# Kernel optimization log

Hardware: AMD Instinct MI355X
Metric: run time of the kernel (lower is better)

## Reference

```python
import jax, jax.numpy as jnp
import numpy as np

N = 100000   # nodes
E = 800000   # edges
P = 100000   # pos/neg pairs
H = 4        # heads
IN = 128     # input feature dim
HID = 32     # per-head out dim (H*HID = 128)


def gat_layer(h, src, dst, W, al, ar, b):
    """DGL-style GATConv: gather -> leaky_relu attention -> segment softmax -> scatter."""
    n = h.shape[0]
    nh, nf = al.shape
    feat = (h @ W).reshape(n, nh, nf)                       # [N,H,F]
    el = jnp.einsum('nhf,hf->nh', feat, al)                 # [N,H]
    er = jnp.einsum('nhf,hf->nh', feat, ar)                 # [N,H]
    e = jax.nn.leaky_relu(el[src] + er[dst], negative_slope=0.2)  # [E,H]
    emax = jax.ops.segment_max(e, dst, num_segments=n)      # [N,H]
    emax = jnp.where(jnp.isfinite(emax), emax, 0.0)         # zero-in-degree guard
    w = jnp.exp(e - emax[dst])                              # [E,H]
    denom = jax.ops.segment_sum(w, dst, num_segments=n)     # [N,H]
    alpha = w / jnp.maximum(denom[dst], 1e-9)               # [E,H]
    out = jax.ops.segment_sum(feat[src] * alpha[:, :, None], dst, num_segments=n)  # [N,H,F]
    return out.reshape(n, nh * nf) + b


def setup_inputs() -> dict:
    key = jax.random.key(0)
    ks = jax.random.split(key, 32)
    s = 0.1
    d = {
        'x': jax.random.normal(ks[0], (N, IN), jnp.float32),
        'src': jax.random.randint(ks[1], (E,), 0, N),
        'dst': jax.random.randint(ks[2], (E,), 0, N),
        'pos_src': jax.random.randint(ks[3], (P,), 0, N),
        'pos_dst': jax.random.randint(ks[4], (P,), 0, N),
        'neg_src': jax.random.randint(ks[5], (P,), 0, N),
        'neg_dst': jax.random.randint(ks[6], (P,), 0, N),
    }
    HF = H * HID
    # 3 GATConv layers, all 128 -> 4x32
    for l in range(3):
        ind = IN if l == 0 else HF
        d[f'W{l}'] = s * jax.random.normal(ks[7 + 4 * l], (ind, HF), jnp.float32)
        d[f'al{l}'] = s * jax.random.normal(ks[8 + 4 * l], (H, HID), jnp.float32)
        d[f'ar{l}'] = s * jax.random.normal(ks[9 + 4 * l], (H, HID), jnp.float32)
        d[f'b{l}'] = jnp.zeros((HF,), jnp.float32)
    # projection 128 -> 32
    d['Wp'] = s * jax.random.normal(ks[20], (HF, HID), jnp.float32)
    d['bp'] = jnp.zeros((HID,), jnp.float32)
    # predictor MLP 32 -> 32 -> 32 -> 1
    d['Wq1'] = s * jax.random.normal(ks[21], (HID, HID), jnp.float32)
    d['bq1'] = jnp.zeros((HID,), jnp.float32)
    d['Wq2'] = s * jax.random.normal(ks[22], (HID, HID), jnp.float32)
    d['bq2'] = jnp.zeros((HID,), jnp.float32)
    d['Wq3'] = s * jax.random.normal(ks[23], (HID, 1), jnp.float32)
    d['bq3'] = jnp.zeros((1,), jnp.float32)
    return d


def reference(x, src, dst, pos_src, pos_dst, neg_src, neg_dst,
              W0, al0, ar0, b0, W1, al1, ar1, b1, W2, al2, ar2, b2,
              Wp, bp, Wq1, bq1, Wq2, bq2, Wq3, bq3):
    h = x
    for W, al, ar, b in ((W0, al0, ar0, b0), (W1, al1, ar1, b1), (W2, al2, ar2, b2)):
        h = jax.nn.elu(gat_layer(h, src, dst, W, al, ar, b))
    h = h @ Wp + bp                                          # [N,HID]

    def predictor(z):
        z = jax.nn.relu(z @ Wq1 + bq1)
        z = jax.nn.relu(z @ Wq2 + bq2)
        return z @ Wq3 + bq3

    h_pos = predictor(h[pos_src] * h[pos_dst])               # [P,1]
    h_neg = predictor(h[neg_src] * h[neg_dst])               # [P,1]
    return (h_pos, h_neg)
```

## Files before the change

kernel.cpp:

```cpp
#include <hip/hip_runtime.h>
#include <math.h>

typedef __attribute__((ext_vector_type(8))) short bf16x8;
typedef __attribute__((ext_vector_type(4))) float f32x4;

__device__ __forceinline__ unsigned short f2bf_rtne(float v) {
    unsigned u = __float_as_uint(v);
    u += 0x7FFFu + ((u >> 16) & 1u);
    return (unsigned short)(u >> 16);
}

__global__ __launch_bounds__(256) void hist_k(const int* __restrict__ dst, int* __restrict__ deg, int e) {
    int i4 = (blockIdx.x * 256 + threadIdx.x) * 4;
    if (i4 + 3 < e) {
        int4 d = *(const int4*)(dst + i4);
        atomicAdd(&deg[d.x], 1);
        atomicAdd(&deg[d.y], 1);
        atomicAdd(&deg[d.z], 1);
        atomicAdd(&deg[d.w], 1);
    } else {
        for (int j = i4; j < e; j++) atomicAdd(&deg[dst[j]], 1);
    }
}

__global__ __launch_bounds__(256) void scan1_k(const int* __restrict__ deg, int* __restrict__ rowptr,
                                               int* __restrict__ bsum, int n) {
    __shared__ int sh[256];
    int tid = threadIdx.x;
    int sid = blockIdx.x * 256 + tid;
    int v = (sid < n) ? deg[sid] : 0;
    sh[tid] = v; __syncthreads();
    for (int off = 1; off < 256; off <<= 1) {
        int t = (tid >= off) ? sh[tid - off] : 0;
        __syncthreads();
        sh[tid] += t;
        __syncthreads();
    }
    if (sid < n) rowptr[sid + 1] = sh[tid];
    if (tid == 255) bsum[blockIdx.x] = sh[255];
}

__global__ __launch_bounds__(512) void scan2_k(int* __restrict__ bsum, int nb) {
    __shared__ int sh[512];
    int tid = threadIdx.x;
    sh[tid] = (tid < nb) ? bsum[tid] : 0;
    __syncthreads();
    for (int off = 1; off < 512; off <<= 1) {
        int t = (tid >= off) ? sh[tid - off] : 0;
        __syncthreads();
        sh[tid] += t;
        __syncthreads();
    }
    if (tid < nb) bsum[tid] = sh[tid];
}

__global__ __launch_bounds__(256) void scan3_k(int* __restrict__ rowptr, int* __restrict__ cursor,
                                               const int* __restrict__ bsum, int n) {
    int sid = blockIdx.x * 256 + threadIdx.x;
    if (sid == 0) { rowptr[0] = 0; cursor[0] = 0; }
    if (sid < n) {
        int v = rowptr[sid + 1];
        if (blockIdx.x > 0) v += bsum[blockIdx.x - 1];
        rowptr[sid + 1] = v;
        cursor[sid + 1] = v;
    }
}

__global__ __launch_bounds__(256) void fill_k(const int* __restrict__ src, const int* __restrict__ dst,
                                              int* __restrict__ cursor, int* __restrict__ csrc, int e) {
    int i4 = (blockIdx.x * 256 + threadIdx.x) * 4;
    if (i4 + 3 < e) {
        int4 s = *(const int4*)(src + i4);
        int4 d = *(const int4*)(dst + i4);
        int p0 = atomicAdd(&cursor[d.x], 1);
        int p1 = atomicAdd(&cursor[d.y], 1);
        int p2 = atomicAdd(&cursor[d.z], 1);
        int p3 = atomicAdd(&cursor[d.w], 1);
        csrc[p0] = s.x; csrc[p1] = s.y; csrc[p2] = s.z; csrc[p3] = s.w;
    } else {
        for (int j = i4; j < e; j++) {
            int pos = atomicAdd(&cursor[dst[j]], 1);
            csrc[pos] = src[j];
        }
    }
}

__global__ __launch_bounds__(256) void wconv3_k(const float* __restrict__ W0, const float* __restrict__ W1,
                                                const float* __restrict__ W2, unsigned short* __restrict__ Bp) {
    int gidx = blockIdx.x * 256 + threadIdx.x;
    int layer = gidx >> 14;
    int idx = gidx & 16383;
    const float* W = (layer == 0) ? W0 : (layer == 1) ? W1 : W2;
    int k = idx >> 7, nc = idx & 127;
    float v = W[idx];
    unsigned short h = f2bf_rtne(v);
    float hf = __uint_as_float((unsigned)h << 16);
    unsigned short lo = f2bf_rtne(v - hf);
    int n = nc >> 4, l15 = nc & 15, ks = k >> 5, lhi = (k >> 3) & 3, j = k & 7;
    int lanei = lhi * 16 + l15;
    unsigned short* B = Bp + (size_t)layer * 32768;
    B[(((ks * 16 + 2 * n) * 64) + lanei) * 8 + j] = h;
    B[(((ks * 16 + 2 * n + 1) * 64) + lanei) * 8 + j] = lo;
}

__global__ __launch_bounds__(512) void gemm_mfma_k(const float* __restrict__ A,
        const unsigned short* __restrict__ Bp,
        const float* __restrict__ alp, const float* __restrict__ arp,
        float* __restrict__ C, float* __restrict__ el, float* __restrict__ er, int M) {
    __shared__ short Bs[4][16][64][8];
    int tid = threadIdx.x;
    int wv = tid >> 6, lane = tid & 63;
    int l15 = lane & 15, lhi = lane >> 4;
    int mb = blockIdx.x * 128 + wv * 16;

    {
        const char* g = (const char*)Bp;
        char* sbase = (char*)&Bs[0][0][0][0];
        #pragma unroll
        for (int p = 0; p < 8; p++) {
            __builtin_amdgcn_global_load_lds(
                (const __attribute__((address_space(1))) unsigned int*)(g + (size_t)(tid + p * 512) * 16),
                (__attribute__((address_space(3))) unsigned int*)(sbase + (wv * 64 + p * 512) * 16),
                16, 0, 0);
        }
    }

    const float* a0p = A + (size_t)min(mb + l15, M - 1) * 128 + lhi * 8;
    float4 A0[4][2];
    #pragma unroll
    for (int ks = 0; ks < 4; ks++) {
        A0[ks][0] = *(const float4*)(a0p + ks * 32);
        A0[ks][1] = *(const float4*)(a0p + ks * 32 + 4);
    }

    f32x4 acc[8];
    #pragma unroll
    for (int n = 0; n < 8; n++) acc[n] = (f32x4){0.f, 0.f, 0.f, 0.f};

    float alv[8], arv[8];
    #pragma unroll
    for (int n = 0; n < 8; n++) { alv[n] = alp[n * 16 + l15]; arv[n] = arp[n * 16 + l15]; }

    __syncthreads();

    #pragma unroll
    for (int ks = 0; ks < 4; ks++) {
        float av[8];
        bf16x8 a0h, a0l;
        *(float4*)(av)     = A0[ks][0];
        *(float4*)(av + 4) = A0[ks][1];
        #pragma unroll
        for (int j = 0; j < 8; j++) {
            unsigned short h = f2bf_rtne(av[j]);
            a0h[j] = (short)h;
            a0l[j] = (short)f2bf_rtne(av[j] - __uint_as_float((unsigned)h << 16));
        }
        const bf16x8* bsv = (const bf16x8*)&Bs[ks][0][0][0];
        #pragma unroll
        for (int n = 0; n < 8; n++) {
            bf16x8 bhv = bsv[(2 * n) * 64 + lane];
            bf16x8 blv = bsv[(2 * n + 1) * 64 + lane];
            acc[n] = __builtin_amdgcn_mfma_f32_16x16x32_bf16(a0h, bhv, acc[n], 0, 0, 0);
            acc[n] = __builtin_amdgcn_mfma_f32_16x16x32_bf16(a0l, bhv, acc[n], 0, 0, 0);
            acc[n] = __builtin_amdgcn_mfma_f32_16x16x32_bf16(a0h, blv, acc[n], 0, 0, 0);
        }
    }

    #pragma unroll
    for (int i = 0; i < 4; i++) {
        int r = mb + lhi * 4 + i;
        bool ok = (r < M);
        if (ok) {
            #pragma unroll
            for (int n = 0; n < 8; n++)
                C[(size_t)r * 128 + n * 16 + l15] = acc[n][i];
        }
        float ph[4], qh[4];
        #pragma unroll
        for (int h = 0; h < 4; h++) {
            ph[h] = acc[2 * h][i] * alv[2 * h] + acc[2 * h + 1][i] * alv[2 * h + 1];
            qh[h] = acc[2 * h][i] * arv[2 * h] + acc[2 * h + 1][i] * arv[2 * h + 1];
        }
        #pragma unroll
        for (int off = 1; off < 16; off <<= 1) {
            #pragma unroll
            for (int h = 0; h < 4; h++) {
                ph[h] += __shfl_xor(ph[h], off);
                qh[h] += __shfl_xor(qh[h], off);
            }
        }
        if (ok && l15 < 8) {
            if (l15 < 4) {
                float v = (l15 == 0) ? ph[0] : (l15 == 1) ? ph[1] : (l15 == 2) ? ph[2] : ph[3];
                el[(size_t)r * 4 + l15] = v;
            } else {
                int h = l15 - 4;
                float v = (h == 0) ? qh[0] : (h == 1) ? qh[1] : (h == 2) ? qh[2] : qh[3];
                er[(size_t)r * 4 + h] = v;
            }
        }
    }
}

__global__ __launch_bounds__(256) void aggregate_k(const float* __restrict__ feat, const float* __restrict__ el,
                                                   const float* __restrict__ er, const int* __restrict__ rowptr,
                                                   const int* __restrict__ csrc, const float* __restrict__ bias,
                                                   float* __restrict__ out, int n) {
    int wid = threadIdx.x >> 6;
    int lane = threadIdx.x & 63;
    int node = blockIdx.x * 4 + wid;
    if (node >= n) return;
    int h = lane >> 4;
    int p0 = rowptr[node], p1 = rowptr[node + 1];
    float erv = er[(size_t)node * 4 + h];
    float2 b2 = *(const float2*)(bias + lane * 2);
    float lsum = 0.f, a0 = 0.f, a1 = 0.f;
    int p = p0;
    for (; p + 8 <= p1; p += 8) {
        int s[8];
        float e[8];
        float2 f[8];
        #pragma unroll
        for (int q = 0; q < 8; q++) s[q] = csrc[p + q];
        #pragma unroll
        for (int q = 0; q < 8; q++) e[q] = el[(size_t)s[q] * 4 + h] + erv;
        #pragma unroll
        for (int q = 0; q < 8; q++) f[q] = *(const float2*)(feat + (size_t)s[q] * 128 + lane * 2);
        #pragma unroll
        for (int q = 0; q < 8; q++) {
            float eq = (e[q] > 0.f) ? e[q] : 0.2f * e[q];
            float w = __expf(eq);
            lsum += w;
            a0 += w * f[q].x;
            a1 += w * f[q].y;
        }
    }
    for (; p + 4 <= p1; p += 4) {
        int s0 = csrc[p], s1 = csrc[p + 1], s2 = csrc[p + 2], s3 = csrc[p + 3];
        float e0 = el[(size_t)s0 * 4 + h] + erv;
        float e1 = el[(size_t)s1 * 4 + h] + erv;
        float e2 = el[(size_t)s2 * 4 + h] + erv;
        float e3 = el[(size_t)s3 * 4 + h] + erv;
        e0 = (e0 > 0.f) ? e0 : 0.2f * e0;
        e1 = (e1 > 0.f) ? e1 : 0.2f * e1;
        e2 = (e2 > 0.f) ? e2 : 0.2f * e2;
        e3 = (e3 > 0.f) ? e3 : 0.2f * e3;
        float2 f0 = *(const float2*)(feat + (size_t)s0 * 128 + lane * 2);
        float2 f1 = *(const float2*)(feat + (size_t)s1 * 128 + lane * 2);
        float2 f2 = *(const float2*)(feat + (size_t)s2 * 128 + lane * 2);
        float2 f3 = *(const float2*)(feat + (size_t)s3 * 128 + lane * 2);
        float w0 = __expf(e0), w1 = __expf(e1), w2 = __expf(e2), w3 = __expf(e3);
        lsum += (w0 + w1) + (w2 + w3);
        a0 += w0 * f0.x + w1 * f1.x + w2 * f2.x + w3 * f3.x;
        a1 += w0 * f0.y + w1 * f1.y + w2 * f2.y + w3 * f3.y;
    }
    for (; p < p1; ++p) {
        int s = csrc[p];
        float e = el[(size_t)s * 4 + h] + erv;
        e = (e > 0.f) ? e : 0.2f * e;
        float w = __expf(e);
        float2 f = *(const float2*)(feat + (size_t)s * 128 + lane * 2);
        lsum += w;
        a0 += w * f.x;
        a1 += w * f.y;
    }
    float inv = 1.f / fmaxf(lsum, 1e-9f);
    float v0 = a0 * inv + b2.x;
    float v1 = a1 * inv + b2.y;
    v0 = (v0 > 0.f) ? v0 : expm1f(v0);
    v1 = (v1 > 0.f) ? v1 : expm1f(v1);
    *(float2*)(out + (size_t)node * 128 + lane * 2) = make_float2(v0, v1);
}

__global__ __launch_bounds__(256) void proj_k(const float* __restrict__ h, const float* __restrict__ Wp,
                                              const float* __restrict__ bp, float* __restrict__ hp, int n) {
    __shared__ float Ws[128 * 32];
    __shared__ float Hs[32][132];
    int tid = threadIdx.x;
    for (int i = tid; i < 4096; i += 256) Ws[i] = Wp[i];
    int n0 = blockIdx.x * 32;
    for (int i = tid; i < 1024; i += 256) {
        int r = i >> 5, c4 = i & 31;
        int node = n0 + r;
        float4 v = (node < n) ? *(const float4*)(h + (size_t)node * 128 + c4 * 4)
                              : make_float4(0.f, 0.f, 0.f, 0.f);
        *(float4*)&Hs[r][c4 * 4] = v;
    }
    __syncthreads();
    int r = tid >> 3;
    int node = n0 + r;
    int j0 = (tid & 7) * 4;
    if (node < n) {
        float a0 = bp[j0], a1 = bp[j0 + 1], a2 = bp[j0 + 2], a3 = bp[j0 + 3];
        #pragma unroll
        for (int k = 0; k < 128; k++) {
            float av = Hs[r][k];
            float4 w = *(const float4*)&Ws[k * 32 + j0];
            a0 += av * w.x; a1 += av * w.y; a2 += av * w.z; a3 += av * w.w;
        }
        *(float4*)(hp + (size_t)node * 32 + j0) = make_float4(a0, a1, a2, a3);
    }
}

__global__ __launch_bounds__(256) void predictor_k(const float* __restrict__ hp,
                                                   const int* __restrict__ ps, const int* __restrict__ pd,
                                                   const int* __restrict__ ns, const int* __restrict__ nd,
                                                   const float* __restrict__ Wq1, const float* __restrict__ bq1,
                                                   const float* __restrict__ Wq2, const float* __restrict__ bq2,
                                                   const float* __restrict__ Wq3, const float* __restrict__ bq3,
                                                   float* __restrict__ out, int P) {
    __shared__ float w1[1024], w2[1024], w3[32], b1[32], b2[32];
    int tid = threadIdx.x;
    for (int i = tid; i < 1024; i += 256) { w1[i] = Wq1[i]; w2[i] = Wq2[i]; }
    if (tid < 32) { w3[tid] = Wq3[tid]; b1[tid] = bq1[tid]; b2[tid] = bq2[tid]; }
    __syncthreads();
    int gid = blockIdx.x * 256 + tid;
    if (gid >= 2 * P) return;
    int i = (gid < P) ? gid : gid - P;
    int a = (gid < P) ? ps[i] : ns[i];
    int b = (gid < P) ? pd[i] : nd[i];
    float z[32];
    const float4* ha = (const float4*)(hp + (size_t)a * 32);
    const float4* hb = (const float4*)(hp + (size_t)b * 32);
    #pragma unroll
    for (int q = 0; q < 8; q++) {
        float4 x = ha[q], y = hb[q];
        z[q * 4 + 0] = x.x * y.x; z[q * 4 + 1] = x.y * y.y;
        z[q * 4 + 2] = x.z * y.z; z[q * 4 + 3] = x.w * y.w;
    }
    float z1[32];
    #pragma unroll
    for (int j = 0; j < 32; j++) {
        float s = b1[j];
        #pragma unroll
        for (int k = 0; k < 32; k++) s += z[k] * w1[k * 32 + j];
        z1[j] = fmaxf(s, 0.f);
    }
    #pragma unroll
    for (int j = 0; j < 32; j++) {
        float s = b2[j];
        #pragma unroll
        for (int k = 0; k < 32; k++) s += z1[k] * w2[k * 32 + j];
        z[j] = fmaxf(s, 0.f);
    }
    float s3 = bq3[0];
    #pragma unroll
    for (int j = 0; j < 32; j++) s3 += z[j] * w3[j];
    out[gid] = s3;
}

extern "C" void kernel_launch(void* const* d_in, const int* in_sizes, int n_in,
                              void* d_out, int out_size, void* d_ws, size_t ws_size,
                              hipStream_t stream) {
    const float* x   = (const float*)d_in[0];
    const int* src   = (const int*)d_in[1];
    const int* dst   = (const int*)d_in[2];
    const int* psrc  = (const int*)d_in[3];
    const int* pdst  = (const int*)d_in[4];
    const int* nsrc  = (const int*)d_in[5];
    const int* ndst  = (const int*)d_in[6];
    const float* W[3]  = { (const float*)d_in[7],  (const float*)d_in[11], (const float*)d_in[15] };
    const float* al[3] = { (const float*)d_in[8],  (const float*)d_in[12], (const float*)d_in[16] };
    const float* ar[3] = { (const float*)d_in[9],  (const float*)d_in[13], (const float*)d_in[17] };
    const float* bb[3] = { (const float*)d_in[10], (const float*)d_in[14], (const float*)d_in[18] };
    const float* Wp  = (const float*)d_in[19];
    const float* bp  = (const float*)d_in[20];
    const float* Wq1 = (const float*)d_in[21];
    const float* bq1 = (const float*)d_in[22];
    const float* Wq2 = (const float*)d_in[23];
    const float* bq2 = (const float*)d_in[24];
    const float* Wq3 = (const float*)d_in[25];
    const float* bq3 = (const float*)d_in[26];
    float* out = (float*)d_out;

    const int N = in_sizes[0] / 128;
    const int E = in_sizes[1];
    const int P = in_sizes[3];

    size_t off = 0;
    auto alloc = [&](size_t bytes) {
        void* p = (char*)d_ws + off;
        off += (bytes + 255) & ~(size_t)255;
        return p;
    };
    float* bufF  = (float*)alloc((size_t)N * 128 * 4);
    float* bufH  = (float*)alloc((size_t)N * 128 * 4);
    float* elA   = (float*)alloc((size_t)N * 4 * 4);
    float* erA   = (float*)alloc((size_t)N * 4 * 4);
    float* hp    = (float*)alloc((size_t)N * 32 * 4);
    int* rowptr  = (int*)alloc((size_t)(N + 1) * 4);
    int* cursor  = (int*)alloc((size_t)(N + 1) * 4);
    int* csrc    = (int*)alloc((size_t)E * 4);
    int* deg     = (int*)alloc((size_t)N * 4);
    int* bsum    = (int*)alloc(1024 * 4);
    unsigned short* Bp = (unsigned short*)alloc(3 * 32768 * 2);
    (void)ws_size;

    const int NB_E4 = (E / 4 + 255) / 256;
    const int NB_N = (N + 255) / 256;

    hipMemsetAsync(deg, 0, (size_t)N * 4, stream);

    hist_k<<<NB_E4, 256, 0, stream>>>(dst, deg, E);
    scan1_k<<<NB_N, 256, 0, stream>>>(deg, rowptr, bsum, N);
    scan2_k<<<1, 512, 0, stream>>>(bsum, NB_N);
    scan3_k<<<NB_N, 256, 0, stream>>>(rowptr, cursor, bsum, N);
    fill_k<<<NB_E4, 256, 0, stream>>>(src, dst, cursor, csrc, E);
    wconv3_k<<<192, 256, 0, stream>>>(W[0], W[1], W[2], Bp);

    const int GEMM_B = (N + 127) / 128;
    const float* hin = x;
    for (int l = 0; l < 3; l++) {
        gemm_mfma_k<<<GEMM_B, 512, 0, stream>>>(hin, Bp + (size_t)l * 32768, al[l], ar[l], bufF, elA, erA, N);
        aggregate_k<<<(N + 3) / 4, 256, 0, stream>>>(bufF, elA, erA, rowptr, csrc, bb[l], bufH, N);
        hin = bufH;
    }
    proj_k<<<(N + 31) / 32, 256, 0, stream>>>(bufH, Wp, bp, hp, N);
    predictor_k<<<(2 * P + 255) / 256, 256, 0, stream>>>(hp, psrc, pdst, nsrc, ndst,
                                                         Wq1, bq1, Wq2, bq2, Wq3, bq3, out, P);
}
```

Measured before the change: 453.5 us.

## Split GEMM columns across wave pairs and double-buffer B in shared memory

Each block now handles 64 rows, with pairs of waves splitting the 8 output column tiles in half. The B operand is streamed through shared memory one K-slice at a time, using two 16KB buffers instead of all 64KB at once. This cuts LDS use and registers per thread to allow more resident blocks, and the launch-bounds hint asks for 8 waves per EU. In exchange, each A row is loaded and converted to split bf16 twice (once per wave in the pair), and a barrier is added per K-step.

```diff
diff --git a/kernel.cpp b/kernel.cpp
--- a/kernel.cpp
+++ b/kernel.cpp
@@ -103,101 +103,106 @@
     B[(((ks * 16 + 2 * n + 1) * 64) + lanei) * 8 + j] = lo;
 }
 
-__global__ __launch_bounds__(512) void gemm_mfma_k(const float* __restrict__ A,
+__global__ __launch_bounds__(512, 8) void gemm_mfma_k(const float* __restrict__ A,
         const unsigned short* __restrict__ Bp,
         const float* __restrict__ alp, const float* __restrict__ arp,
         float* __restrict__ C, float* __restrict__ el, float* __restrict__ er, int M) {
-    __shared__ short Bs[4][16][64][8];
+    __shared__ short Bs[2][16][64][8];
     int tid = threadIdx.x;
     int wv = tid >> 6, lane = tid & 63;
     int l15 = lane & 15, lhi = lane >> 4;
-    int mb = blockIdx.x * 128 + wv * 16;
+    int nhalf = wv & 1;
+    int mb = blockIdx.x * 64 + (wv >> 1) * 16;
+
+    const float* ap = A + (size_t)min(mb + l15, M - 1) * 128 + lhi * 8;
 
     {
         const char* g = (const char*)Bp;
-        char* sbase = (char*)&Bs[0][0][0][0];
-        #pragma unroll
-        for (int p = 0; p < 8; p++) {
+        char* sb = (char*)&Bs[0][0][0][0];
+        #pragma unroll
+        for (int p = 0; p < 2; p++) {
             __builtin_amdgcn_global_load_lds(
                 (const __attribute__((address_space(1))) unsigned int*)(g + (size_t)(tid + p * 512) * 16),
-                (__attribute__((address_space(3))) unsigned int*)(sbase + (wv * 64 + p * 512) * 16),
+                (__attribute__((address_space(3))) unsigned int*)(sb + p * 8192 + wv * 1024),
                 16, 0, 0);
         }
     }
 
-    const float* a0p = A + (size_t)min(mb + l15, M - 1) * 128 + lhi * 8;
-    float4 A0[4][2];
+    f32x4 acc[4];
+    #pragma unroll
+    for (int j = 0; j < 4; j++) acc[j] = (f32x4){0.f, 0.f, 0.f, 0.f};
+
+    __syncthreads();
+
     #pragma unroll
     for (int ks = 0; ks < 4; ks++) {
-        A0[ks][0] = *(const float4*)(a0p + ks * 32);
-        A0[ks][1] = *(const float4*)(a0p + ks * 32 + 4);
-    }
-
-    f32x4 acc[8];
-    #pragma unroll
-    for (int n = 0; n < 8; n++) acc[n] = (f32x4){0.f, 0.f, 0.f, 0.f};
-
-    float alv[8], arv[8];
-    #pragma unroll
-    for (int n = 0; n < 8; n++) { alv[n] = alp[n * 16 + l15]; arv[n] = arp[n * 16 + l15]; }
-
-    __syncthreads();
-
-    #pragma unroll
-    for (int ks = 0; ks < 4; ks++) {
+        int buf = ks & 1;
+        if (ks < 3) {
+            const char* g = (const char*)Bp + (size_t)(ks + 1) * 16384;
+            char* sb = (char*)&Bs[buf ^ 1][0][0][0];
+            #pragma unroll
+            for (int p = 0; p < 2; p++) {
+                __builtin_amdgcn_global_load_lds(
+                    (const __attribute__((address_space(1))) unsigned int*)(g + (size_t)(tid + p * 512) * 16),
+                    (__attribute__((address_space(3))) unsigned int*)(sb + p * 8192 + wv * 1024),
+                    16, 0, 0);
+            }
+        }
         float av[8];
-        bf16x8 a0h, a0l;
-        *(float4*)(av)     = A0[ks][0];
-        *(float4*)(av + 4) = A0[ks][1];
+        bf16x8 ah, alo;
+        *(float4*)(av)     = *(const float4*)(ap + ks * 32);
+        *(float4*)(av + 4) = *(const float4*)(ap + ks * 32 + 4);
         #pragma unroll
         for (int j = 0; j < 8; j++) {
             unsigned short h = f2bf_rtne(av[j]);
-            a0h[j] = (short)h;
-            a0l[j] = (short)f2bf_rtne(av[j] - __uint_as_float((unsigned)h << 16));
-        }
-        const bf16x8* bsv = (const bf16x8*)&Bs[ks][0][0][0];
-        #pragma unroll
-        for (int n = 0; n < 8; n++) {
+            ah[j]  = (short)h;
+            alo[j] = (short)f2bf_rtne(av[j] - __uint_as_float((unsigned)h << 16));
+        }
+        const bf16x8* bsv = (const bf16x8*)&Bs[buf][0][0][0];
+        #pragma unroll
+        for (int j = 0; j < 4; j++) {
+            int n = nhalf * 4 + j;
             bf16x8 bhv = bsv[(2 * n) * 64 + lane];
             bf16x8 blv = bsv[(2 * n + 1) * 64 + lane];
-            acc[n] = __builtin_amdgcn_mfma_f32_16x16x32_bf16(a0h, bhv, acc[n], 0, 0, 0);
-            acc[n] = __builtin_amdgcn_mfma_f32_16x16x32_bf16(a0l, bhv, acc[n], 0, 0, 0);
-            acc[n] = __builtin_amdgcn_mfma_f32_16x16x32_bf16(a0h, blv, acc[n], 0, 0, 0);
-        }
-    }
-
+            acc[j] = __builtin_amdgcn_mfma_f32_16x16x32_bf16(ah,  bhv, acc[j], 0, 0, 0);
+            acc[j] = __builtin_amdgcn_mfma_f32_16x16x32_bf16(alo, bhv, acc[j], 0, 0, 0);
+            acc[j] = __builtin_amdgcn_mfma_f32_16x16x32_bf16(ah,  blv, acc[j], 0, 0, 0);
+        }
+        __syncthreads();
+    }
+
+    float alv[4], arv[4];
+    #pragma unroll
+    for (int j = 0; j < 4; j++) {
+        alv[j] = alp[(nhalf * 4 + j) * 16 + l15];
+        arv[j] = arp[(nhalf * 4 + j) * 16 + l15];
+    }
     #pragma unroll
     for (int i = 0; i < 4; i++) {
         int r = mb + lhi * 4 + i;
         bool ok = (r < M);
         if (ok) {
             #pragma unroll
-            for (int n = 0; n < 8; n++)
-                C[(size_t)r * 128 + n * 16 + l15] = acc[n][i];
-        }
-        float ph[4], qh[4];
-        #pragma unroll
-        for (int h = 0; h < 4; h++) {
-            ph[h] = acc[2 * h][i] * alv[2 * h] + acc[2 * h + 1][i] * alv[2 * h + 1];
-            qh[h] = acc[2 * h][i] * arv[2 * h] + acc[2 * h + 1][i] * arv[2 * h + 1];
-        }
+            for (int j = 0; j < 4; j++)
+                C[(size_t)r * 128 + (nhalf * 4 + j) * 16 + l15] = acc[j][i];
+        }
+        float p0 = acc[0][i] * alv[0] + acc[1][i] * alv[1];
+        float p1 = acc[2][i] * alv[2] + acc[3][i] * alv[3];
+        float q0 = acc[0][i] * arv[0] + acc[1][i] * arv[1];
+        float q1 = acc[2][i] * arv[2] + acc[3][i] * arv[3];
         #pragma unroll
         for (int off = 1; off < 16; off <<= 1) {
-            #pragma unroll
-            for (int h = 0; h < 4; h++) {
-                ph[h] += __shfl_xor(ph[h], off);
-                qh[h] += __shfl_xor(qh[h], off);
-            }
-        }
-        if (ok && l15 < 8) {
-            if (l15 < 4) {
-                float v = (l15 == 0) ? ph[0] : (l15 == 1) ? ph[1] : (l15 == 2) ? ph[2] : ph[3];
-                el[(size_t)r * 4 + l15] = v;
-            } else {
-                int h = l15 - 4;
-                float v = (h == 0) ? qh[0] : (h == 1) ? qh[1] : (h == 2) ? qh[2] : qh[3];
-                er[(size_t)r * 4 + h] = v;
-            }
+            p0 += __shfl_xor(p0, off);
+            p1 += __shfl_xor(p1, off);
+            q0 += __shfl_xor(q0, off);
+            q1 += __shfl_xor(q1, off);
+        }
+        if (ok && l15 < 4) {
+            int base = r * 4 + 2 * nhalf;
+            if (l15 == 0)      el[base]     = p0;
+            else if (l15 == 1) el[base + 1] = p1;
+            else if (l15 == 2) er[base]     = q0;
+            else               er[base + 1] = q1;
         }
     }
 }
@@ -408,7 +413,7 @@
     fill_k<<<NB_E4, 256, 0, stream>>>(src, dst, cursor, csrc, E);
     wconv3_k<<<192, 256, 0, stream>>>(W[0], W[1], W[2], Bp);
 
-    const int GEMM_B = (N + 127) / 128;
+    const int GEMM_B = (N + 63) / 64;
     const float* hin = x;
     for (int l = 0; l < 3; l++) {
         gemm_mfma_k<<<GEMM_B, 512, 0, stream>>>(hin, Bp + (size_t)l * 32768, al[l], ar[l], bufF, elA, erA, N);
```

Measured after the change: 461.5 us. Within noise of the previous version (+1.8%).
